# Kernel tuning notes

Measured on AMD Instinct MI355X. Metric: run time of the kernel, lower is better.

Reference implementation:

```python
import jax, jax.numpy as jnp
import numpy as np

B, L, C, K = 32, 512, 256, 3


def conv1d_1ch(sig, w, b):
    # sig: (B, L) single-channel signal; w: (C, 1, K); b: (C,) -> (B, L, C)
    y = jax.lax.conv_general_dilated(
        sig[:, None, :], w, window_strides=(1,), padding=[((K - 1) // 2, (K - 1) // 2)],
        dimension_numbers=('NCH', 'OIH', 'NCH'))  # (B, C, L)
    return y.transpose(0, 2, 1) + b


def setup_inputs() -> dict:
    keys = jax.random.split(jax.random.key(0), 12)
    x = jax.random.normal(keys[0], (B, L, C), dtype=jnp.float32)
    durations_float = jax.random.uniform(keys[1], (B, L), dtype=jnp.float32) * 8.0
    durations_int = jax.random.randint(keys[2], (B, L), 1, 9)
    energies = jax.random.normal(keys[3], (B, L), dtype=jnp.float32)
    pitch = jax.random.normal(keys[4], (B, L), dtype=jnp.float32)
    input_lengths = jax.random.randint(keys[5], (B,), L // 2, L + 1)
    input_lengths = input_lengths.at[0].set(L)  # ensure max_len == L as in torch mask
    Wd = jax.random.normal(keys[6], (C, 1, K), dtype=jnp.float32) * 0.1
    We = jax.random.normal(keys[7], (C, 1, K), dtype=jnp.float32) * 0.1
    Wp = jax.random.normal(keys[8], (C, 1, K), dtype=jnp.float32) * 0.1
    bd = jnp.zeros((C,), jnp.float32)
    be = jnp.zeros((C,), jnp.float32)
    bp = jnp.zeros((C,), jnp.float32)
    Wproj = jax.random.normal(keys[9], (1, C), dtype=jnp.float32) * 0.05
    bproj = jnp.zeros((1,), jnp.float32)
    return dict(x=x, durations_float=durations_float, energies=energies, pitch=pitch,
                Wd=Wd, bd=bd, We=We, be=be, Wp=Wp, bp=bp, Wproj=Wproj, bproj=bproj,
                durations_int=durations_int, input_lengths=input_lengths)


def reference(x, durations_float, energies, pitch, Wd, bd, We, be, Wp, bp, Wproj, bproj,
              durations_int, input_lengths):
    d = conv1d_1ch(durations_float, Wd, bd)   # (B, L, C)
    e = conv1d_1ch(energies, We, be)          # (B, L, C)
    p = conv1d_1ch(pitch, Wp, bp)             # (B, L, C)
    xc = x + e + p                            # x_combined == x_summed (no concatenation)
    range_inputs = xc + d
    ranges = jax.nn.softplus(range_inputs @ Wproj.T + bproj)[..., 0]  # (B, L)

    pad = jnp.arange(L)[None, :] >= input_lengths[:, None]  # True on padding
    ranges = jnp.where(pad, 1.0, ranges)

    cumsum = jnp.cumsum(durations_int, axis=1)
    means = durations_int.astype(jnp.float32) * 0.5
    means = means + jnp.pad(cumsum[:, :-1], ((0, 0), (1, 0))).astype(jnp.float32)  # (B, L)

    T = int(jnp.max(cumsum))
    frames = jnp.arange(T, dtype=jnp.float32) + 0.5  # (T,)

    # Normal(mean, std).log_prob(frames), then exp
    z = (frames[None, None, :] - means[..., None]) / ranges[..., None]  # (B, L, T)
    log_prob = -0.5 * z * z - jnp.log(ranges)[..., None] - 0.5 * jnp.log(2.0 * jnp.pi)
    probs = jnp.exp(log_prob)
    probs = jnp.where(pad[..., None], 0.0, probs)
    weights = probs / (jnp.sum(probs, axis=1, keepdims=True) + 1e-20)  # (B, L, T)

    # sum over L of (B,L,C,T) broadcast-product, done as a batched contraction
    x_upsamp = jnp.einsum('blc,blt->btc', xc, weights)  # (B, T, C)
    return x_upsamp, weights
```

## Files before the change

### kernel.cpp

```cpp
#include <hip/hip_runtime.h>

#define NB 32
#define NL 512
#define NC 256

typedef __attribute__((ext_vector_type(8))) short short8v;
typedef __attribute__((ext_vector_type(4))) float f32x4;

__device__ __forceinline__ unsigned short f2bf(float x) {
    unsigned int u = __float_as_uint(x);
    return (unsigned short)((u + 0x7FFFu + ((u >> 16) & 1u)) >> 16);
}

__global__ __launch_bounds__(256) void k_xct(
    const float* __restrict__ x,
    const float* __restrict__ energ, const float* __restrict__ pitch,
    const float* __restrict__ We, const float* __restrict__ be,
    const float* __restrict__ Wp, const float* __restrict__ bp,
    const float* __restrict__ Wproj,
    unsigned short* __restrict__ xcT, float* __restrict__ rd)
{
    __shared__ float se[34], sp[34];
    __shared__ float part[4][32];
    int lt = blockIdx.x, b = blockIdx.y;
    int c = threadIdx.x;
    int lane = c & 63, wv = c >> 6;
    int l0 = lt * 32;
    if (c < 34) {
        int gl = l0 - 1 + c;
        bool ok = (gl >= 0) && (gl < NL);
        se[c] = ok ? energ[b*NL + gl] : 0.f;
        sp[c] = ok ? pitch[b*NL + gl] : 0.f;
    }
    __syncthreads();
    float we0 = We[c*3], we1 = We[c*3+1], we2 = We[c*3+2];
    float wp0 = Wp[c*3], wp1 = Wp[c*3+1], wp2 = Wp[c*3+2];
    float bb = be[c] + bp[c];
    float pw = Wproj[c];
    const float* xb = x + ((size_t)b*NL + l0)*NC + c;
    unsigned int w32[16];
#pragma unroll
    for (int l = 0; l < 32; ++l) {
        float conv = we0*se[l] + we1*se[l+1] + we2*se[l+2]
                   + wp0*sp[l] + wp1*sp[l+1] + wp2*sp[l+2] + bb;
        float v = xb[(size_t)l*NC] + conv;
        unsigned int bits = f2bf(v);
        if (l & 1) w32[l>>1] |= bits << 16;
        else       w32[l>>1]  = bits;
        float contrib = v * pw;
#pragma unroll
        for (int off = 32; off > 0; off >>= 1)
            contrib += __shfl_down(contrib, off, 64);
        if (lane == 0) part[wv][l] = contrib;
    }
    uint4* dst = (uint4*)(xcT + ((size_t)(b*16 + lt)*NC + c)*32);
    const uint4* src = (const uint4*)w32;
#pragma unroll
    for (int k = 0; k < 4; ++k) dst[k] = src[k];
    __syncthreads();
    if (c < 32)
        rd[b*NL + l0 + c] = part[0][c] + part[1][c] + part[2][c] + part[3][c];
}

__global__ __launch_bounds__(512) void k_ranges(
    const float* __restrict__ df, const int* __restrict__ di,
    const int* __restrict__ ilen,
    const float* __restrict__ Wd, const float* __restrict__ bd,
    const float* __restrict__ Wproj, const float* __restrict__ bproj,
    const float* __restrict__ rd,
    float* __restrict__ meanO, float* __restrict__ invrO, float* __restrict__ coefO)
{
    __shared__ float r2[4][8];
    __shared__ float pwS[4];
    __shared__ int sbuf[2][NL];
    int b = blockIdx.x;
    int l = threadIdx.x;
    int lane = l & 63, wv = l >> 6;

    float vals[4] = {0.f, 0.f, 0.f, 0.f};
    if (l < 256) {
        float w = Wproj[l];
        vals[0] = Wd[l*3]*w; vals[1] = Wd[l*3+1]*w; vals[2] = Wd[l*3+2]*w;
        vals[3] = bd[l]*w;
    }
#pragma unroll
    for (int q = 0; q < 4; ++q) {
        float v = vals[q];
#pragma unroll
        for (int off = 32; off > 0; off >>= 1) v += __shfl_down(v, off, 64);
        if (lane == 0) r2[q][wv] = v;
    }

    int d = di[b*NL + l];
    sbuf[0][l] = d;
    __syncthreads();
    if (l < 4) {
        float s = 0.f;
#pragma unroll
        for (int w8 = 0; w8 < 8; ++w8) s += r2[l][w8];
        pwS[l] = s;
    }
    int cur = 0;
    for (int off = 1; off < NL; off <<= 1) {
        int v = sbuf[cur][l];
        if (l >= off) v += sbuf[cur][l - off];
        sbuf[cur^1][l] = v;
        __syncthreads();
        cur ^= 1;
    }
    int incl = sbuf[cur][l];
    float mean = (float)incl - 0.5f*(float)d;

    int ro = b*NL + l;
    float fm1 = (l > 0)      ? df[ro-1] : 0.f;
    float f0  =                df[ro];
    float fp1 = (l < NL-1)   ? df[ro+1] : 0.f;
    float rin = rd[ro]
              + pwS[0]*fm1 + pwS[1]*f0 + pwS[2]*fp1
              + pwS[3] + bproj[0];
    float rng = (rin > 20.f) ? rin : log1pf(expf(rin));
    bool pad = (l >= ilen[b]);
    float invr = 1.f / rng;
    meanO[ro] = mean;
    invrO[ro] = pad ? 1.f : invr;
    coefO[ro] = pad ? 0.f : 0.3989422804014327f * invr;
}

__global__ __launch_bounds__(256) void k_fused(
    const unsigned short* __restrict__ xcT,
    const float* __restrict__ meanA, const float* __restrict__ invrA,
    const float* __restrict__ coefA,
    float* __restrict__ outX, float* __restrict__ outW, int T)
{
    __shared__ __align__(16) unsigned short wT[32 * NL];
    __shared__ float red[8][32];
    __shared__ float dinvS[32];
    __shared__ unsigned int fl[16];

    int b = blockIdx.y;
    int t0 = blockIdx.x << 5;
    int tid = threadIdx.x;
    int tcol = tid & 31;
    int lbase = tid >> 5;
    if (tid < 16) fl[tid] = 0u;
    __syncthreads();

    int t = t0 + tcol;
    float fr = (float)t + 0.5f;
    const float* mB = meanA + b*NL;
    const float* iB = invrA + b*NL;
    const float* cB = coefA + b*NL;
    char* wbase = (char*)wT;
    int sw = (tcol & 7) << 4;

    float pv[8][8];
    float partial = 0.f;
#pragma unroll
    for (int i = 0; i < 8; ++i) {
        int ci = lbase + (i << 3);
        int lc = ci << 3;
        const float4 m0  = *(const float4*)(mB + lc);
        const float4 m1  = *(const float4*)(mB + lc + 4);
        const float4 iv0 = *(const float4*)(iB + lc);
        const float4 iv1 = *(const float4*)(iB + lc + 4);
        const float4 cv0 = *(const float4*)(cB + lc);
        const float4 cv1 = *(const float4*)(cB + lc + 4);
        float mm[8] = {m0.x,m0.y,m0.z,m0.w,m1.x,m1.y,m1.z,m1.w};
        float ii[8] = {iv0.x,iv0.y,iv0.z,iv0.w,iv1.x,iv1.y,iv1.z,iv1.w};
        float cc[8] = {cv0.x,cv0.y,cv0.z,cv0.w,cv1.x,cv1.y,cv1.z,cv1.w};
        float sum = 0.f;
#pragma unroll
        for (int j = 0; j < 8; ++j) {
            float z = (fr - mm[j]) * ii[j];
            float z2 = z*z;
            float p = (z2 < 450.f) ? cc[j]*__expf(-0.5f*z2) : 0.f;
            pv[i][j] = p;
            sum += p;
        }
        if (sum > 0.f) fl[ci >> 2] = 1u;
        partial += sum;
    }
    red[lbase][tcol] = partial;
    __syncthreads();
    if (tid < 32) {
        float s = 0.f;
#pragma unroll
        for (int g = 0; g < 8; ++g) s += red[g][tid];
        dinvS[tid] = 1.f / (s + 1e-20f);
    }
    __syncthreads();
    float dv = dinvS[tcol];

    bool tok = t < T;
    float* ow = outW + (size_t)b*NL*T + t;
#pragma unroll
    for (int i = 0; i < 8; ++i) {
        int ci = lbase + (i << 3);
        int lc = ci << 3;
        union { unsigned int u[4]; short8v v; } pk;
#pragma unroll
        for (int j = 0; j < 4; ++j) {
            float w0 = pv[i][2*j]   * dv;
            float w1 = pv[i][2*j+1] * dv;
            pk.u[j] = (unsigned int)f2bf(w0) | ((unsigned int)f2bf(w1) << 16);
            if (tok) {
                ow[(size_t)(lc + 2*j)   * T] = w0;
                ow[(size_t)(lc + 2*j+1) * T] = w1;
            }
        }
        *(short8v*)(wbase + (((tcol << 10) + (ci << 4)) ^ sw)) = pk.v;
    }
    __syncthreads();

    int lane = tid & 63;
    int wvid = tid >> 6;
    int g = lane >> 4;
    int m = lane & 15;
    f32x4 acc[2][4];
#pragma unroll
    for (int mt = 0; mt < 2; ++mt)
#pragma unroll
        for (int nt = 0; nt < 4; ++nt) acc[mt][nt] = (f32x4){0.f,0.f,0.f,0.f};

    const unsigned short* xb = xcT + (size_t)b * 16 * 8192;
    int asw = (m & 7) << 4;

    for (int ks = 0; ks < 16; ++ks) {
        if (fl[ks] == 0u) continue;
        const unsigned short* xk = xb + ks*8192 + g*8;
        short8v a0 = *(const short8v*)(wbase + (((m << 10)      + ks*64 + (g << 4)) ^ asw));
        short8v a1 = *(const short8v*)(wbase + ((((16+m) << 10) + ks*64 + (g << 4)) ^ asw));
#pragma unroll
        for (int nt = 0; nt < 4; ++nt) {
            short8v bf = *(const short8v*)(xk + (size_t)(wvid*64 + nt*16 + m)*32);
            acc[0][nt] = __builtin_amdgcn_mfma_f32_16x16x32_bf16(a0, bf, acc[0][nt], 0, 0, 0);
            acc[1][nt] = __builtin_amdgcn_mfma_f32_16x16x32_bf16(a1, bf, acc[1][nt], 0, 0, 0);
        }
    }

    float* outB = outX + (size_t)b*T*NC + (size_t)(wvid*64 + m);
#pragma unroll
    for (int mt = 0; mt < 2; ++mt) {
#pragma unroll
        for (int r = 0; r < 4; ++r) {
            int tt = t0 + mt*16 + g*4 + r;
            if (tt < T) {
#pragma unroll
                for (int nt = 0; nt < 4; ++nt)
                    outB[(size_t)tt*NC + nt*16] = acc[mt][nt][r];
            }
        }
    }
}

extern "C" void kernel_launch(void* const* d_in, const int* in_sizes, int n_in,
                              void* d_out, int out_size, void* d_ws, size_t ws_size,
                              hipStream_t stream)
{
    const float* x   = (const float*)d_in[0];
    const float* df  = (const float*)d_in[1];
    const float* en  = (const float*)d_in[2];
    const float* pi  = (const float*)d_in[3];
    const float* Wd  = (const float*)d_in[4];
    const float* bd  = (const float*)d_in[5];
    const float* We  = (const float*)d_in[6];
    const float* be  = (const float*)d_in[7];
    const float* Wp  = (const float*)d_in[8];
    const float* bp  = (const float*)d_in[9];
    const float* Wpr = (const float*)d_in[10];
    const float* bpr = (const float*)d_in[11];
    const int*   di  = (const int*)d_in[12];
    const int*   il  = (const int*)d_in[13];

    int T = out_size / (NB * (NC + NL));

    float* outX = (float*)d_out;
    float* outW = outX + (size_t)NB * T * NC;

    float* rdp   = (float*)d_ws;
    float* meanp = rdp   + NB*NL;
    float* invrp = meanp + NB*NL;
    float* coefp = invrp + NB*NL;
    unsigned short* xcT = (unsigned short*)(coefp + NB*NL);

    hipLaunchKernelGGL(k_xct, dim3(16, NB), dim3(256), 0, stream,
                       x, en, pi, We, be, Wp, bp, Wpr, xcT, rdp);
    hipLaunchKernelGGL(k_ranges, dim3(NB), dim3(512), 0, stream,
                       df, di, il, Wd, bd, Wpr, bpr, rdp, meanp, invrp, coefp);
    hipLaunchKernelGGL(k_fused, dim3((T+31)/32, NB), dim3(256), 0, stream,
                       xcT, meanp, invrp, coefp, outX, outW, T);
}
```

Before: 346.0 us.

## Split weight output into separate row-major kernel and skip far-away Gaussian columns

The fused kernel now limits its L-range per time tile by binary-searching the sorted means against a window derived from the per-batch max range. It no longer writes the weights tensor and instead stores the per-frame normalizers. A new kernel writes the weights row by row with coalesced float4-style stores, computing the exponential only inside each row's window and writing zeros elsewhere. This trades recomputing the exponentials and an extra launch for removing the strided column writes and most of the out-of-window exp work. Contributions beyond about 21 standard deviations are treated as exactly zero.

Result: faster. 330.2 us (-4.6%).

```diff
diff --git a/kernel.cpp b/kernel.cpp
--- a/kernel.cpp
+++ b/kernel.cpp
@@ -68,10 +68,12 @@
     const float* __restrict__ Wd, const float* __restrict__ bd,
     const float* __restrict__ Wproj, const float* __restrict__ bproj,
     const float* __restrict__ rd,
-    float* __restrict__ meanO, float* __restrict__ invrO, float* __restrict__ coefO)
+    float* __restrict__ meanO, float* __restrict__ invrO, float* __restrict__ coefO,
+    float* __restrict__ rmaxA)
 {
     __shared__ float r2[4][8];
     __shared__ float pwS[4];
+    __shared__ float rm[8];
     __shared__ int sbuf[2][NL];
     int b = blockIdx.x;
     int l = threadIdx.x;
@@ -124,40 +126,60 @@
     meanO[ro] = mean;
     invrO[ro] = pad ? 1.f : invr;
     coefO[ro] = pad ? 0.f : 0.3989422804014327f * invr;
-}
-
-__global__ __launch_bounds__(256) void k_fused(
+
+    float rv = pad ? 0.f : rng;
+#pragma unroll
+    for (int off = 32; off > 0; off >>= 1)
+        rv = fmaxf(rv, __shfl_down(rv, off, 64));
+    if (lane == 0) rm[wv] = rv;
+    __syncthreads();
+    if (l == 0) {
+        float mx = rm[0];
+#pragma unroll
+        for (int w8 = 1; w8 < 8; ++w8) mx = fmaxf(mx, rm[w8]);
+        rmaxA[b] = mx;
+    }
+}
+
+__global__ __launch_bounds__(256) void k_gemmx(
     const unsigned short* __restrict__ xcT,
     const float* __restrict__ meanA, const float* __restrict__ invrA,
-    const float* __restrict__ coefA,
-    float* __restrict__ outX, float* __restrict__ outW, int T)
+    const float* __restrict__ coefA, const float* __restrict__ rmaxA,
+    float* __restrict__ outX, float* __restrict__ dinvA, int T)
 {
     __shared__ __align__(16) unsigned short wT[32 * NL];
     __shared__ float red[8][32];
     __shared__ float dinvS[32];
     __shared__ unsigned int fl[16];
+    __shared__ int rngS[2];
 
     int b = blockIdx.y;
     int t0 = blockIdx.x << 5;
     int tid = threadIdx.x;
     int tcol = tid & 31;
     int lbase = tid >> 5;
-    if (tid < 16) fl[tid] = 0u;
-    __syncthreads();
-
-    int t = t0 + tcol;
-    float fr = (float)t + 0.5f;
     const float* mB = meanA + b*NL;
     const float* iB = invrA + b*NL;
     const float* cB = coefA + b*NL;
+    if (tid < 16) fl[tid] = 0u;
+    if (tid == 0) {
+        float span = 21.25f * rmaxA[b] + 1.0f;
+        float A = (float)t0 + 0.5f - span;
+        float Bv = (float)(t0 + 31) + 0.5f + span;
+        int lo = 0, hi = 0;
+        for (int s = 256; s; s >>= 1) if (lo + s <= NL && mB[lo + s - 1] <  A ) lo += s;
+        for (int s = 256; s; s >>= 1) if (hi + s <= NL && mB[hi + s - 1] <= Bv) hi += s;
+        rngS[0] = (lo >> 5) << 2;
+        rngS[1] = ((hi + 31) >> 5) << 2;
+    }
+    __syncthreads();
+    int sc0 = rngS[0], sc1 = rngS[1];
+    float fr = (float)(t0 + tcol) + 0.5f;
     char* wbase = (char*)wT;
     int sw = (tcol & 7) << 4;
 
-    float pv[8][8];
     float partial = 0.f;
-#pragma unroll
-    for (int i = 0; i < 8; ++i) {
-        int ci = lbase + (i << 3);
+    for (int ci = sc0 + lbase; ci < sc1; ci += 8) {
         int lc = ci << 3;
         const float4 m0  = *(const float4*)(mB + lc);
         const float4 m1  = *(const float4*)(mB + lc + 4);
@@ -173,9 +195,7 @@
         for (int j = 0; j < 8; ++j) {
             float z = (fr - mm[j]) * ii[j];
             float z2 = z*z;
-            float p = (z2 < 450.f) ? cc[j]*__expf(-0.5f*z2) : 0.f;
-            pv[i][j] = p;
-            sum += p;
+            sum += (z2 < 450.f) ? cc[j]*__expf(-0.5f*z2) : 0.f;
         }
         if (sum > 0.f) fl[ci >> 2] = 1u;
         partial += sum;
@@ -186,27 +206,34 @@
         float s = 0.f;
 #pragma unroll
         for (int g = 0; g < 8; ++g) s += red[g][tid];
-        dinvS[tid] = 1.f / (s + 1e-20f);
+        float dvv = 1.f / (s + 1e-20f);
+        dinvS[tid] = dvv;
+        int t = t0 + tid;
+        if (t < T) dinvA[(size_t)b*T + t] = dvv;
     }
     __syncthreads();
     float dv = dinvS[tcol];
 
-    bool tok = t < T;
-    float* ow = outW + (size_t)b*NL*T + t;
-#pragma unroll
-    for (int i = 0; i < 8; ++i) {
-        int ci = lbase + (i << 3);
+    for (int ci = sc0 + lbase; ci < sc1; ci += 8) {
         int lc = ci << 3;
+        const float4 m0  = *(const float4*)(mB + lc);
+        const float4 m1  = *(const float4*)(mB + lc + 4);
+        const float4 iv0 = *(const float4*)(iB + lc);
+        const float4 iv1 = *(const float4*)(iB + lc + 4);
+        const float4 cv0 = *(const float4*)(cB + lc);
+        const float4 cv1 = *(const float4*)(cB + lc + 4);
+        float mm[8] = {m0.x,m0.y,m0.z,m0.w,m1.x,m1.y,m1.z,m1.w};
+        float ii[8] = {iv0.x,iv0.y,iv0.z,iv0.w,iv1.x,iv1.y,iv1.z,iv1.w};
+        float cc[8] = {cv0.x,cv0.y,cv0.z,cv0.w,cv1.x,cv1.y,cv1.z,cv1.w};
         union { unsigned int u[4]; short8v v; } pk;
 #pragma unroll
         for (int j = 0; j < 4; ++j) {
-            float w0 = pv[i][2*j]   * dv;
-            float w1 = pv[i][2*j+1] * dv;
+            float z0 = (fr - mm[2*j])   * ii[2*j];
+            float z1 = (fr - mm[2*j+1]) * ii[2*j+1];
+            float q0 = z0*z0, q1 = z1*z1;
+            float w0 = (q0 < 450.f) ? cc[2*j]  *__expf(-0.5f*q0)*dv : 0.f;
+            float w1 = (q1 < 450.f) ? cc[2*j+1]*__expf(-0.5f*q1)*dv : 0.f;
             pk.u[j] = (unsigned int)f2bf(w0) | ((unsigned int)f2bf(w1) << 16);
-            if (tok) {
-                ow[(size_t)(lc + 2*j)   * T] = w0;
-                ow[(size_t)(lc + 2*j+1) * T] = w1;
-            }
         }
         *(short8v*)(wbase + (((tcol << 10) + (ci << 4)) ^ sw)) = pk.v;
     }
@@ -248,6 +275,61 @@
 #pragma unroll
                 for (int nt = 0; nt < 4; ++nt)
                     outB[(size_t)tt*NC + nt*16] = acc[mt][nt][r];
+            }
+        }
+    }
+}
+
+__global__ __launch_bounds__(256) void k_weightsC(
+    const float* __restrict__ meanA, const float* __restrict__ invrA,
+    const float* __restrict__ coefA, const float* __restrict__ dinvA,
+    float* __restrict__ outW, int T)
+{
+    __shared__ float sm[32], si[32], sc[32];
+    __shared__ int wlo[32], whi[32];
+    int lt = blockIdx.x, b = blockIdx.y;
+    int tid = threadIdx.x;
+    int l0 = lt * 32;
+    if (tid < 32) {
+        float m  = meanA[b*NL + l0 + tid];
+        float iv = invrA[b*NL + l0 + tid];
+        float cf = coefA[b*NL + l0 + tid];
+        sm[tid] = m; si[tid] = iv; sc[tid] = cf;
+        float span = 21.25f / iv + 1.0f;
+        int a  = (int)floorf(m - span);
+        int b2 = (int)ceilf(m + span) + 1;
+        if (cf == 0.f) { a = 0; b2 = 0; }
+        wlo[tid] = max(0, a);
+        whi[tid] = min(T, b2);
+    }
+    __syncthreads();
+    const float* dB = dinvA + (size_t)b*T;
+    float* ow = outW + ((size_t)b*NL + l0)*T;
+    int nch = (T + 1023) >> 10;
+    for (int l = 0; l < 32; ++l) {
+        float m = sm[l], iv = si[l], cf = sc[l];
+        int lo = wlo[l], hi = whi[l];
+        float* row = ow + (size_t)l*T;
+        for (int ch = 0; ch < nch; ++ch) {
+            int t4 = (ch << 10) + (tid << 2);
+            if (t4 >= T) break;
+            float v0 = 0.f, v1 = 0.f, v2 = 0.f, v3 = 0.f;
+            if (t4 + 4 > lo && t4 < hi) {
+                float f0v = (float)t4 + 0.5f;
+                float z;
+                z = (f0v        - m)*iv; v0 = (z*z < 450.f) ? cf*__expf(-0.5f*z*z)*dB[t4]   : 0.f;
+                if (t4+1 < T) { z = (f0v+1.f - m)*iv; v1 = (z*z < 450.f) ? cf*__expf(-0.5f*z*z)*dB[t4+1] : 0.f; }
+                if (t4+2 < T) { z = (f0v+2.f - m)*iv; v2 = (z*z < 450.f) ? cf*__expf(-0.5f*z*z)*dB[t4+2] : 0.f; }
+                if (t4+3 < T) { z = (f0v+3.f - m)*iv; v3 = (z*z < 450.f) ? cf*__expf(-0.5f*z*z)*dB[t4+3] : 0.f; }
+            }
+            if (t4 + 4 <= T) {
+                row[t4]   = v0; row[t4+1] = v1;
+                row[t4+2] = v2; row[t4+3] = v3;
+            } else {
+                row[t4] = v0;
+                if (t4+1 < T) row[t4+1] = v1;
+                if (t4+2 < T) row[t4+2] = v2;
+                if (t4+3 < T) row[t4+3] = v3;
             }
         }
     }
@@ -277,16 +359,20 @@
     float* outX = (float*)d_out;
     float* outW = outX + (size_t)NB * T * NC;
 
-    float* rdp   = (float*)d_ws;
+    unsigned short* xcT = (unsigned short*)d_ws;
+    float* rdp   = (float*)(xcT + (size_t)NB*16*NC*32);
     float* meanp = rdp   + NB*NL;
     float* invrp = meanp + NB*NL;
     float* coefp = invrp + NB*NL;
-    unsigned short* xcT = (unsigned short*)(coefp + NB*NL);
+    float* dinvp = coefp + NB*NL;
+    float* rmaxp = dinvp + (size_t)NB*T;
 
     hipLaunchKernelGGL(k_xct, dim3(16, NB), dim3(256), 0, stream,
                        x, en, pi, We, be, Wp, bp, Wpr, xcT, rdp);
     hipLaunchKernelGGL(k_ranges, dim3(NB), dim3(512), 0, stream,
-                       df, di, il, Wd, bd, Wpr, bpr, rdp, meanp, invrp, coefp);
-    hipLaunchKernelGGL(k_fused, dim3((T+31)/32, NB), dim3(256), 0, stream,
-                       xcT, meanp, invrp, coefp, outX, outW, T);
-}
+                       df, di, il, Wd, bd, Wpr, bpr, rdp, meanp, invrp, coefp, rmaxp);
+    hipLaunchKernelGGL(k_gemmx, dim3((T+31)/32, NB), dim3(256), 0, stream,
+                       xcT, meanp, invrp, coefp, rmaxp, outX, dinvp, T);
+    hipLaunchKernelGGL(k_weightsC, dim3(16, NB), dim3(256), 0, stream,
+                       meanp, invrp, coefp, dinvp, outW, T);
+}
```
